# Kernel optimization log

Hardware: AMD Instinct MI355X
Metric: run time of the kernel (lower is better)

Reference implementation:

```python
import jax, jax.numpy as jnp
import numpy as np

N_NODES = 50000
N_EDGES = 1000000
H_DIM = 128
OUT_DIM = 64
N_RELS = 16  # num_bases == num_rels


def setup_inputs() -> dict:
    key = jax.random.key(0)
    ks = jax.random.split(key, 12)
    node_ids = jnp.arange(N_NODES, dtype=jnp.int64) if jax.config.jax_enable_x64 else jnp.arange(N_NODES, dtype=jnp.int32)
    src = jax.random.randint(ks[0], (N_EDGES,), 0, N_NODES)
    dst = jax.random.randint(ks[1], (N_EDGES,), 0, N_NODES)
    etype = jax.random.randint(ks[2], (N_EDGES,), 0, N_RELS)
    norm = jax.random.uniform(ks[3], (N_EDGES, 1), dtype=jnp.float32)
    s1 = 1.0 / np.sqrt(H_DIM)
    s2 = 1.0 / np.sqrt(OUT_DIM)
    emb = jax.random.normal(ks[4], (N_NODES, H_DIM), dtype=jnp.float32)
    V1 = jax.random.normal(ks[5], (N_RELS, H_DIM, H_DIM), dtype=jnp.float32) * s1
    comp1 = jax.random.normal(ks[6], (N_RELS, N_RELS), dtype=jnp.float32) * (1.0 / np.sqrt(N_RELS))
    bias1 = jnp.zeros((H_DIM,), dtype=jnp.float32)
    V2 = jax.random.normal(ks[7], (N_RELS, H_DIM, OUT_DIM), dtype=jnp.float32) * s2
    comp2 = jax.random.normal(ks[8], (N_RELS, N_RELS), dtype=jnp.float32) * (1.0 / np.sqrt(N_RELS))
    bias2 = jnp.zeros((OUT_DIM,), dtype=jnp.float32)
    return {"node_ids": node_ids, "src": src, "dst": dst, "etype": etype, "norm": norm,
            "emb": emb, "V1": V1, "comp1": comp1, "bias1": bias1,
            "V2": V2, "comp2": comp2, "bias2": bias2}


def _rel_graph_conv(x, src, dst, etype, norm, V, comp, bias, num_nodes):
    # Basis decomposition: W_r = sum_b comp[r, b] * V_b  -> [R, in, out]
    W = jnp.einsum('rb,bio->rio', comp, V)
    # Per-relation transform of all nodes: [R, N, out]
    Y = jnp.einsum('ni,rio->rno', x, W)
    # Per-edge message: gather (etype, src) then scale by norm  -> [E, out]
    m = Y[etype, src] * norm
    # Scatter-add to destination nodes
    h = jax.ops.segment_sum(m, dst, num_segments=num_nodes)
    return h + bias


def reference(node_ids, src, dst, etype, norm, emb, V1, comp1, bias1, V2, comp2, bias2):
    x = emb[node_ids]  # [N, H]
    h = jax.nn.relu(_rel_graph_conv(x, src, dst, etype, norm, V1, comp1, bias1, x.shape[0]))
    h = _rel_graph_conv(h, src, dst, etype, norm, V2, comp2, bias2, x.shape[0])
    return h
```

## Files before the change

kernel.cpp:

```cpp
#include <hip/hip_runtime.h>


typedef short bf16x8 __attribute__((ext_vector_type(8)));
typedef float f32x4 __attribute__((ext_vector_type(4)));

#define RELS 16
#define HDIM 128
#define DSTBLK 66
#define MT_P 5
#define CHUNK 32
#define MAXBINS 12288
#define MAXCH 96

__device__ inline unsigned short f2bf(float f) {
  unsigned int u = __float_as_uint(f);
  unsigned int r = u + 0x7FFFu + ((u >> 16) & 1u);
  return (unsigned short)(r >> 16);
}

__device__ inline void barrier_nodrain() {
  __builtin_amdgcn_sched_barrier(0);
  asm volatile("s_waitcnt lgkmcnt(0)" ::: "memory");
  __builtin_amdgcn_s_barrier();
  __builtin_amdgcn_sched_barrier(0);
}

__global__ void cvt_bf16(const float* __restrict__ in, unsigned short* __restrict__ out, int n8) {
  int i = blockIdx.x * blockDim.x + threadIdx.x;
  if (i >= n8) return;
  float4 a = ((const float4*)in)[i * 2];
  float4 b = ((const float4*)in)[i * 2 + 1];
  uint4 o;
  o.x = (unsigned)f2bf(a.x) | ((unsigned)f2bf(a.y) << 16);
  o.y = (unsigned)f2bf(a.z) | ((unsigned)f2bf(a.w) << 16);
  o.z = (unsigned)f2bf(b.x) | ((unsigned)f2bf(b.y) << 16);
  o.w = (unsigned)f2bf(b.z) | ((unsigned)f2bf(b.w) << 16);
  ((uint4*)out)[i] = o;
}

__global__ void compute_w(const float* __restrict__ comp, const float* __restrict__ V,
                          unsigned short* __restrict__ Wt, int IO) {
  int idx = blockIdx.x * blockDim.x + threadIdx.x;
  if (idx >= RELS * IO * HDIM) return;
  int k = idx & (HDIM - 1);
  int o = (idx >> 7) % IO;
  int r = idx / (IO * HDIM);
  float s = 0.f;
#pragma unroll
  for (int b = 0; b < RELS; b++)
    s = fmaf(comp[r * RELS + b], V[(size_t)b * HDIM * IO + (size_t)k * IO + o], s);
  Wt[idx] = f2bf(s);
}

__global__ void hist_bins(const int* __restrict__ dst, const int* __restrict__ etype,
                          int n, int nbins, int* __restrict__ counts) {
  __shared__ int lh[MAXBINS];
  for (int j = threadIdx.x; j < nbins; j += blockDim.x) lh[j] = 0;
  __syncthreads();
  for (int i = blockIdx.x * blockDim.x + threadIdx.x; i < n; i += gridDim.x * blockDim.x)
    atomicAdd(&lh[(dst[i] / DSTBLK) * RELS + etype[i]], 1);
  __syncthreads();
  for (int j = threadIdx.x; j < nbins; j += blockDim.x) {
    int c = lh[j];
    if (c) atomicAdd(&counts[j], c);
  }
}

__global__ void scan_offsets(const int* __restrict__ counts, int* __restrict__ offsets, int nbins) {
  __shared__ int csum[256];
  const int t = threadIdx.x;
  const int CH = (nbins + 255) / 256;
  int lo = t * CH, hi = min(lo + CH, nbins);
  int s = 0;
  for (int i = lo; i < hi; i++) s += (counts[i] + 15) & ~15;
  csum[t] = s;
  __syncthreads();
#pragma unroll
  for (int d = 1; d < 256; d <<= 1) {
    int v = (t >= d) ? csum[t - d] : 0;
    __syncthreads();
    csum[t] += v;
    __syncthreads();
  }
  int run = (t == 0) ? 0 : csum[t - 1];
  for (int i = lo; i < hi; i++) {
    offsets[i] = run;
    run += (counts[i] + 15) & ~15;
  }
  if (lo < nbins && hi == nbins) offsets[nbins] = run;
}

__global__ void scatter_bins(const int* __restrict__ src, const int* __restrict__ dst,
                             const int* __restrict__ etype, const float* __restrict__ norm,
                             int n, const int* __restrict__ offsets, int* __restrict__ cursor,
                             uint2* __restrict__ ebuf) {
  for (int i = blockIdx.x * blockDim.x + threadIdx.x; i < n; i += gridDim.x * blockDim.x) {
    int d = dst[i];
    int blk = d / DSTBLK;
    int b = blk * RELS + etype[i];
    int p = offsets[b] + atomicAdd(&cursor[b], 1);
    ebuf[p] = make_uint2((unsigned)src[i] | ((unsigned)(d - blk * DSTBLK) << 20),
                         __float_as_uint(norm[i]));
  }
}

template <int OUT, bool BF16_RELU_OUT>
__launch_bounds__(256, 3)
__global__ void rgcn_layer(const unsigned short* __restrict__ Xb,
                           const unsigned short* __restrict__ Wt,
                           const uint2* __restrict__ ebuf,
                           const int* __restrict__ offsets, const int* __restrict__ counts,
                           const float* __restrict__ bias, void* __restrict__ Hout,
                           int nNodes) {
  constexpr int NT = OUT / 64;
  __shared__ __align__(16) unsigned short xs[2][CHUNK][136];
  __shared__ __align__(16) unsigned short ys[OUT][40];
  __shared__ __align__(16) unsigned short pmat[2][80][40];
  __shared__ __align__(16) int4 descS[MAXCH];
  __shared__ int sBase[16], sCnt[16], sStart[17];

  const int t = threadIdx.x;
  const int w = t >> 6;
  const int lane = t & 63;
  const int quad = lane >> 4;
  const int l16 = lane & 15;
  const int r0 = t >> 4;
  const int k8 = t & 15;
  const bool isHandler = (t & 7) == 0;
  const int myCol = t >> 3;
  const int nodeBase = blockIdx.x * DSTBLK;
  const int binBase = blockIdx.x * RELS;
  const int colBase = w * (OUT / 4);

  for (int i = t; i < 2 * CHUNK * 136 / 8; i += 256) ((uint4*)xs)[i] = make_uint4(0, 0, 0, 0);
  for (int i = t; i < OUT * 40 / 8; i += 256) ((uint4*)ys)[i] = make_uint4(0, 0, 0, 0);
  for (int i = t; i < 2 * 80 * 40 / 8; i += 256) ((uint4*)pmat)[i] = make_uint4(0, 0, 0, 0);

  if (t < 16) {
    sBase[t] = offsets[binBase + t];
    sCnt[t] = counts[binBase + t];
  }
  __syncthreads();
  if (t == 0) {
    int run = 0;
#pragma unroll
    for (int b = 0; b < 16; b++) {
      sStart[b] = run;
      run += (sCnt[b] + CHUNK - 1) / CHUNK;
    }
    sStart[16] = min(run, MAXCH);
  }
  __syncthreads();
  if (t < 16) {
    int st = sStart[t], ba = sBase[t], c = sCnt[t];
    for (int j = 0; j * CHUNK < c; j++)
      if (st + j < MAXCH)
        descS[st + j] = make_int4(ba + j * CHUNK, min(CHUNK, c - j * CHUNK), t, 0);
  }
  __syncthreads();
  const int nCh = sStart[16];

  f32x4 pacc[MT_P][NT] = {};

  uint2 EnE0, EnE1, EnEm;
  uint2 En2E0, En2E1, En2Em;
  uint4 GnG0, GnG1;
  int n1 = 0, n2 = 0;
  int pdA = -1, pdB = -1;

  if (nCh > 0) {
    int4 d0 = descS[0];
    int4 d1 = (nCh > 1) ? descS[1] : make_int4(0, 0, 0, 0);
    int4 d2 = (nCh > 2) ? descS[2] : make_int4(0, 0, 0, 0);
    n1 = d1.y;
    n2 = d2.y;
    uint2 a0, a1, am;
    if (r0 < d0.y) a0 = ebuf[d0.x + r0];
    if (16 + r0 < d0.y) a1 = ebuf[d0.x + 16 + r0];
    if (isHandler && myCol < d0.y) am = ebuf[d0.x + myCol];
    if (r0 < n1) EnE0 = ebuf[d1.x + r0];
    if (16 + r0 < n1) EnE1 = ebuf[d1.x + 16 + r0];
    if (isHandler && myCol < n1) EnEm = ebuf[d1.x + myCol];
    if (r0 < n2) En2E0 = ebuf[d2.x + r0];
    if (16 + r0 < n2) En2E1 = ebuf[d2.x + 16 + r0];
    if (isHandler && myCol < n2) En2Em = ebuf[d2.x + myCol];
    if (r0 < d0.y)
      *(uint4*)&xs[0][r0][k8 * 8] =
          *(const uint4*)(Xb + (size_t)(a0.x & 0xFFFFFu) * HDIM + k8 * 8);
    if (16 + r0 < d0.y)
      *(uint4*)&xs[0][16 + r0][k8 * 8] =
          *(const uint4*)(Xb + (size_t)(a1.x & 0xFFFFFu) * HDIM + k8 * 8);
    if (isHandler && myCol < d0.y) {
      int dl = (int)(am.x >> 20) & 127;
      pmat[0][dl][myCol] = f2bf(__uint_as_float(am.y));
      pdB = dl;
    }
    if (r0 < n1) GnG0 = *(const uint4*)(Xb + (size_t)(EnE0.x & 0xFFFFFu) * HDIM + k8 * 8);
    if (16 + r0 < n1) GnG1 = *(const uint4*)(Xb + (size_t)(EnE1.x & 0xFFFFFu) * HDIM + k8 * 8);
  }
  barrier_nodrain();

  int cb = 0;
  int curRel = -1;
  bf16x8 wf[4][NT];

  for (int ci = 0; ci < nCh; ci++) {
    int4 dc = descS[ci];
    const int nRows = dc.y;

    if (dc.z != curRel) {
      curRel = dc.z;
      const unsigned short* Wr = Wt + (size_t)curRel * OUT * HDIM;
#pragma unroll
      for (int ks = 0; ks < 4; ks++)
#pragma unroll
        for (int nt = 0; nt < NT; nt++)
          wf[ks][nt] = *(const bf16x8*)(Wr + (size_t)(colBase + nt * 16 + l16) * HDIM + ks * 32 + quad * 8);
    }

    int4 d3 = make_int4(0, 0, 0, 0);
    if (ci + 3 < nCh) d3 = descS[ci + 3];
    uint2 EwE0, EwE1, EwEm;
    if (r0 < d3.y) EwE0 = ebuf[d3.x + r0];
    if (16 + r0 < d3.y) EwE1 = ebuf[d3.x + 16 + r0];
    if (isHandler && myCol < d3.y) EwEm = ebuf[d3.x + myCol];

#pragma unroll
    for (int mt = 0; mt < 2; mt++) {
      if (mt * 16 < nRows) {
        f32x4 dacc[NT] = {};
        __builtin_amdgcn_s_setprio(1);
#pragma unroll
        for (int ks = 0; ks < 4; ks++) {
          bf16x8 a = *(const bf16x8*)&xs[cb][mt * 16 + l16][ks * 32 + quad * 8];
#pragma unroll
          for (int nt = 0; nt < NT; nt++)
            dacc[nt] = __builtin_amdgcn_mfma_f32_16x16x32_bf16(a, wf[ks][nt], dacc[nt], 0, 0, 0);
        }
        __builtin_amdgcn_s_setprio(0);
#pragma unroll
        for (int nt = 0; nt < NT; nt++) {
          uint2 pk;
          pk.x = (unsigned)f2bf(dacc[nt][0]) | ((unsigned)f2bf(dacc[nt][1]) << 16);
          pk.y = (unsigned)f2bf(dacc[nt][2]) | ((unsigned)f2bf(dacc[nt][3]) << 16);
          *(uint2*)&ys[colBase + nt * 16 + l16][mt * 16 + quad * 4] = pk;
        }
      }
    }

    uint4 GwG0, GwG1;
    if (r0 < n2) GwG0 = *(const uint4*)(Xb + (size_t)(En2E0.x & 0xFFFFFu) * HDIM + k8 * 8);
    if (16 + r0 < n2) GwG1 = *(const uint4*)(Xb + (size_t)(En2E1.x & 0xFFFFFu) * HDIM + k8 * 8);

    {
      bf16x8 bfv[NT];
#pragma unroll
      for (int nt = 0; nt < NT; nt++)
        bfv[nt] = *(const bf16x8*)&ys[colBase + nt * 16 + l16][quad * 8];
      __builtin_amdgcn_s_setprio(1);
#pragma unroll
      for (int mt = 0; mt < MT_P; mt++) {
        bf16x8 a = *(const bf16x8*)&pmat[cb][mt * 16 + l16][quad * 8];
#pragma unroll
        for (int nt = 0; nt < NT; nt++)
          pacc[mt][nt] = __builtin_amdgcn_mfma_f32_16x16x32_bf16(a, bfv[nt], pacc[mt][nt], 0, 0, 0);
      }
      __builtin_amdgcn_s_setprio(0);
    }

    if (r0 < n1) *(uint4*)&xs[cb ^ 1][r0][k8 * 8] = GnG0;
    if (16 + r0 < n1) *(uint4*)&xs[cb ^ 1][16 + r0][k8 * 8] = GnG1;
    if (isHandler) {
      if (pdA >= 0) pmat[cb ^ 1][pdA][myCol] = 0;
      if (myCol < n1) {
        int dl = (int)(EnEm.x >> 20) & 127;
        pmat[cb ^ 1][dl][myCol] = f2bf(__uint_as_float(EnEm.y));
        pdA = dl;
      } else {
        pdA = -1;
      }
    }
    { int tmp = pdA; pdA = pdB; pdB = tmp; }

    EnE0 = En2E0; EnE1 = En2E1; EnEm = En2Em;
    En2E0 = EwE0; En2E1 = EwE1; En2Em = EwEm;
    GnG0 = GwG0; GnG1 = GwG1;
    n1 = n2; n2 = d3.y;

    if (ci + 1 < nCh) barrier_nodrain();
    cb ^= 1;
  }

#pragma unroll
  for (int mt = 0; mt < MT_P; mt++) {
#pragma unroll
    for (int reg = 0; reg < 4; reg++) {
      int ld = mt * 16 + quad * 4 + reg;
      int node = nodeBase + ld;
      if (ld < DSTBLK && node < nNodes) {
#pragma unroll
        for (int nt = 0; nt < NT; nt++) {
          int col = colBase + nt * 16 + l16;
          float v = pacc[mt][nt][reg] + bias[col];
          if constexpr (BF16_RELU_OUT)
            ((unsigned short*)Hout)[(size_t)node * OUT + col] = f2bf(fmaxf(v, 0.f));
          else
            ((float*)Hout)[(size_t)node * OUT + col] = v;
        }
      }
    }
  }
}

extern "C" void kernel_launch(void* const* d_in, const int* in_sizes, int n_in,
                              void* d_out, int out_size, void* d_ws, size_t ws_size,
                              hipStream_t stream) {
  const int*   src   = (const int*)d_in[1];
  const int*   dst   = (const int*)d_in[2];
  const int*   etype = (const int*)d_in[3];
  const float* norm  = (const float*)d_in[4];
  const float* emb   = (const float*)d_in[5];
  const float* V1    = (const float*)d_in[6];
  const float* comp1 = (const float*)d_in[7];
  const float* bias1 = (const float*)d_in[8];
  const float* V2    = (const float*)d_in[9];
  const float* comp2 = (const float*)d_in[10];
  const float* bias2 = (const float*)d_in[11];
  float* out = (float*)d_out;

  const int N = in_sizes[0];
  const int E = in_sizes[1];
  const int H = 128, O = 64;
  const int NB = (N + DSTBLK - 1) / DSTBLK;
  const int NBINS = NB * RELS;
  const int EPAD_MAX = E + NBINS * 16;

  char* ws = (char*)d_ws;
  size_t off = 0;
  auto alloc = [&](size_t bytes) -> void* {
    void* p = ws + off;
    off += (bytes + 255) & ~(size_t)255;
    return p;
  };
  unsigned short* W1t  = (unsigned short*)alloc(sizeof(short) * RELS * H * H);
  unsigned short* W2t  = (unsigned short*)alloc(sizeof(short) * RELS * O * H);
  unsigned short* embh = (unsigned short*)alloc(sizeof(short) * (size_t)N * H);
  unsigned short* h1b  = (unsigned short*)alloc(sizeof(short) * (size_t)N * H);
  uint2* ebuf = (uint2*)alloc(sizeof(uint2) * EPAD_MAX);
  int* counts  = (int*)alloc(sizeof(int) * NBINS);
  int* cursor  = (int*)alloc(sizeof(int) * NBINS);
  int* offsets = (int*)alloc(sizeof(int) * (NBINS + 1));

  hipMemsetAsync(counts, 0, sizeof(int) * NBINS, stream);
  hipMemsetAsync(cursor, 0, sizeof(int) * NBINS, stream);

  cvt_bf16<<<((size_t)N * H / 8 + 255) / 256, 256, 0, stream>>>(emb, embh, N * H / 8);
  compute_w<<<(RELS * H * H + 255) / 256, 256, 0, stream>>>(comp1, V1, W1t, H);
  compute_w<<<(RELS * O * H + 255) / 256, 256, 0, stream>>>(comp2, V2, W2t, O);
  hist_bins<<<256, 256, 0, stream>>>(dst, etype, E, NBINS, counts);
  scan_offsets<<<1, 256, 0, stream>>>(counts, offsets, NBINS);
  scatter_bins<<<1024, 256, 0, stream>>>(src, dst, etype, norm, E, offsets, cursor, ebuf);

  rgcn_layer<128, true><<<NB, 256, 0, stream>>>(embh, W1t, ebuf, offsets, counts, bias1, (void*)h1b, N);
  rgcn_layer<64, false><<<NB, 256, 0, stream>>>(h1b, W2t, ebuf, offsets, counts, bias2, (void*)out, N);
}
```

Measured before the change: 420.4 us.

## Replace scatter-matrix MFMA with LDS float atomics for per-edge accumulation

The kernel no longer builds a bf16 one-hot norm matrix and runs a second MFMA to scatter per-edge messages onto destination nodes. It keeps the per-edge transform results in registers and adds them, scaled by norm, into an fp32 LDS output tile with shared-memory atomics. The output tile is then written out with vectorized stores that fold in bias and ReLU. Together with the launch-bounds change this drops the zero-initialisation and bf16 round trip of the intermediate and keeps fp32 accumulation, at the cost of many LDS atomics and possible contention on popular destinations.

Measured after the change: 1.334 ms. 217% more time.

```diff
diff --git a/kernel.cpp b/kernel.cpp
--- a/kernel.cpp
+++ b/kernel.cpp
@@ -7,7 +7,6 @@
 #define RELS 16
 #define HDIM 128
 #define DSTBLK 66
-#define MT_P 5
 #define CHUNK 32
 #define MAXBINS 12288
 #define MAXCH 96
@@ -105,7 +104,7 @@
 }
 
 template <int OUT, bool BF16_RELU_OUT>
-__launch_bounds__(256, 3)
+__launch_bounds__(256, (OUT == 64) ? 4 : 3)
 __global__ void rgcn_layer(const unsigned short* __restrict__ Xb,
                            const unsigned short* __restrict__ Wt,
                            const uint2* __restrict__ ebuf,
@@ -113,10 +112,12 @@
                            const float* __restrict__ bias, void* __restrict__ Hout,
                            int nNodes) {
   constexpr int NT = OUT / 64;
+  constexpr int OSTR = OUT + 4;
   __shared__ __align__(16) unsigned short xs[2][CHUNK][136];
-  __shared__ __align__(16) unsigned short ys[OUT][40];
-  __shared__ __align__(16) unsigned short pmat[2][80][40];
-  __shared__ __align__(16) int4 descS[MAXCH];
+  __shared__ __align__(16) float lds_out[DSTBLK * OSTR];
+  __shared__ __align__(16) float normS[2][CHUNK];
+  __shared__ __align__(4) unsigned char dlocS[2][CHUNK];
+  __shared__ __align__(8) int2 descS[MAXCH];
   __shared__ int sBase[16], sCnt[16], sStart[17];
 
   const int t = threadIdx.x;
@@ -126,15 +127,11 @@
   const int l16 = lane & 15;
   const int r0 = t >> 4;
   const int k8 = t & 15;
-  const bool isHandler = (t & 7) == 0;
-  const int myCol = t >> 3;
   const int nodeBase = blockIdx.x * DSTBLK;
   const int binBase = blockIdx.x * RELS;
   const int colBase = w * (OUT / 4);
 
-  for (int i = t; i < 2 * CHUNK * 136 / 8; i += 256) ((uint4*)xs)[i] = make_uint4(0, 0, 0, 0);
-  for (int i = t; i < OUT * 40 / 8; i += 256) ((uint4*)ys)[i] = make_uint4(0, 0, 0, 0);
-  for (int i = t; i < 2 * 80 * 40 / 8; i += 256) ((uint4*)pmat)[i] = make_uint4(0, 0, 0, 0);
+  for (int i = t; i < DSTBLK * OSTR / 4; i += 256) ((uint4*)lds_out)[i] = make_uint4(0, 0, 0, 0);
 
   if (t < 16) {
     sBase[t] = offsets[binBase + t];
@@ -155,45 +152,45 @@
     int st = sStart[t], ba = sBase[t], c = sCnt[t];
     for (int j = 0; j * CHUNK < c; j++)
       if (st + j < MAXCH)
-        descS[st + j] = make_int4(ba + j * CHUNK, min(CHUNK, c - j * CHUNK), t, 0);
+        descS[st + j] = make_int2(ba + j * CHUNK, min(CHUNK, c - j * CHUNK) | (t << 8));
   }
   __syncthreads();
   const int nCh = sStart[16];
 
-  f32x4 pacc[MT_P][NT] = {};
-
-  uint2 EnE0, EnE1, EnEm;
-  uint2 En2E0, En2E1, En2Em;
+  uint2 EnE0, EnE1;
+  uint2 En2E0, En2E1;
   uint4 GnG0, GnG1;
   int n1 = 0, n2 = 0;
-  int pdA = -1, pdB = -1;
 
   if (nCh > 0) {
-    int4 d0 = descS[0];
-    int4 d1 = (nCh > 1) ? descS[1] : make_int4(0, 0, 0, 0);
-    int4 d2 = (nCh > 2) ? descS[2] : make_int4(0, 0, 0, 0);
-    n1 = d1.y;
-    n2 = d2.y;
-    uint2 a0, a1, am;
-    if (r0 < d0.y) a0 = ebuf[d0.x + r0];
-    if (16 + r0 < d0.y) a1 = ebuf[d0.x + 16 + r0];
-    if (isHandler && myCol < d0.y) am = ebuf[d0.x + myCol];
+    int2 d0 = descS[0];
+    int2 d1 = (nCh > 1) ? descS[1] : make_int2(0, 0);
+    int2 d2 = (nCh > 2) ? descS[2] : make_int2(0, 0);
+    const int rows0 = d0.y & 0xFF;
+    n1 = d1.y & 0xFF;
+    n2 = d2.y & 0xFF;
+    uint2 a0, a1;
+    if (r0 < rows0) a0 = ebuf[d0.x + r0];
+    if (16 + r0 < rows0) a1 = ebuf[d0.x + 16 + r0];
     if (r0 < n1) EnE0 = ebuf[d1.x + r0];
     if (16 + r0 < n1) EnE1 = ebuf[d1.x + 16 + r0];
-    if (isHandler && myCol < n1) EnEm = ebuf[d1.x + myCol];
     if (r0 < n2) En2E0 = ebuf[d2.x + r0];
     if (16 + r0 < n2) En2E1 = ebuf[d2.x + 16 + r0];
-    if (isHandler && myCol < n2) En2Em = ebuf[d2.x + myCol];
-    if (r0 < d0.y)
+    if (r0 < rows0) {
       *(uint4*)&xs[0][r0][k8 * 8] =
           *(const uint4*)(Xb + (size_t)(a0.x & 0xFFFFFu) * HDIM + k8 * 8);
-    if (16 + r0 < d0.y)
+      if (k8 == 0) {
+        dlocS[0][r0] = (unsigned char)((a0.x >> 20) & 127u);
+        normS[0][r0] = __uint_as_float(a0.y);
+      }
+    }
+    if (16 + r0 < rows0) {
       *(uint4*)&xs[0][16 + r0][k8 * 8] =
           *(const uint4*)(Xb + (size_t)(a1.x & 0xFFFFFu) * HDIM + k8 * 8);
-    if (isHandler && myCol < d0.y) {
-      int dl = (int)(am.x >> 20) & 127;
-      pmat[0][dl][myCol] = f2bf(__uint_as_float(am.y));
-      pdB = dl;
+      if (k8 == 0) {
+        dlocS[0][16 + r0] = (unsigned char)((a1.x >> 20) & 127u);
+        normS[0][16 + r0] = __uint_as_float(a1.y);
+      }
     }
     if (r0 < n1) GnG0 = *(const uint4*)(Xb + (size_t)(EnE0.x & 0xFFFFFu) * HDIM + k8 * 8);
     if (16 + r0 < n1) GnG1 = *(const uint4*)(Xb + (size_t)(EnE1.x & 0xFFFFFu) * HDIM + k8 * 8);
@@ -205,12 +202,13 @@
   bf16x8 wf[4][NT];
 
   for (int ci = 0; ci < nCh; ci++) {
-    int4 dc = descS[ci];
-    const int nRows = dc.y;
-
-    if (dc.z != curRel) {
-      curRel = dc.z;
-      const unsigned short* Wr = Wt + (size_t)curRel * OUT * HDIM;
+    int2 dc = descS[ci];
+    const int nRows = dc.y & 0xFF;
+    const int rel = dc.y >> 8;
+
+    if (rel != curRel) {
+      curRel = rel;
+      const unsigned short* Wr = Wt + (size_t)rel * OUT * HDIM;
 #pragma unroll
       for (int ks = 0; ks < 4; ks++)
 #pragma unroll
@@ -218,33 +216,28 @@
           wf[ks][nt] = *(const bf16x8*)(Wr + (size_t)(colBase + nt * 16 + l16) * HDIM + ks * 32 + quad * 8);
     }
 
-    int4 d3 = make_int4(0, 0, 0, 0);
+    int2 d3 = make_int2(0, 0);
     if (ci + 3 < nCh) d3 = descS[ci + 3];
-    uint2 EwE0, EwE1, EwEm;
-    if (r0 < d3.y) EwE0 = ebuf[d3.x + r0];
-    if (16 + r0 < d3.y) EwE1 = ebuf[d3.x + 16 + r0];
-    if (isHandler && myCol < d3.y) EwEm = ebuf[d3.x + myCol];
-
+    const int rows3 = d3.y & 0xFF;
+    uint2 EwE0, EwE1;
+    if (r0 < rows3) EwE0 = ebuf[d3.x + r0];
+    if (16 + r0 < rows3) EwE1 = ebuf[d3.x + 16 + r0];
+
+    f32x4 dacc[2][NT];
 #pragma unroll
     for (int mt = 0; mt < 2; mt++) {
+#pragma unroll
+      for (int nt = 0; nt < NT; nt++) dacc[mt][nt] = (f32x4){0.f, 0.f, 0.f, 0.f};
       if (mt * 16 < nRows) {
-        f32x4 dacc[NT] = {};
         __builtin_amdgcn_s_setprio(1);
 #pragma unroll
         for (int ks = 0; ks < 4; ks++) {
           bf16x8 a = *(const bf16x8*)&xs[cb][mt * 16 + l16][ks * 32 + quad * 8];
 #pragma unroll
           for (int nt = 0; nt < NT; nt++)
-            dacc[nt] = __builtin_amdgcn_mfma_f32_16x16x32_bf16(a, wf[ks][nt], dacc[nt], 0, 0, 0);
+            dacc[mt][nt] = __builtin_amdgcn_mfma_f32_16x16x32_bf16(a, wf[ks][nt], dacc[mt][nt], 0, 0, 0);
         }
         __builtin_amdgcn_s_setprio(0);
-#pragma unroll
-        for (int nt = 0; nt < NT; nt++) {
-          uint2 pk;
-          pk.x = (unsigned)f2bf(dacc[nt][0]) | ((unsigned)f2bf(dacc[nt][1]) << 16);
-          pk.y = (unsigned)f2bf(dacc[nt][2]) | ((unsigned)f2bf(dacc[nt][3]) << 16);
-          *(uint2*)&ys[colBase + nt * 16 + l16][mt * 16 + quad * 4] = pk;
-        }
       }
     }
 
@@ -252,61 +245,76 @@
     if (r0 < n2) GwG0 = *(const uint4*)(Xb + (size_t)(En2E0.x & 0xFFFFFu) * HDIM + k8 * 8);
     if (16 + r0 < n2) GwG1 = *(const uint4*)(Xb + (size_t)(En2E1.x & 0xFFFFFu) * HDIM + k8 * 8);
 
-    {
-      bf16x8 bfv[NT];
-#pragma unroll
-      for (int nt = 0; nt < NT; nt++)
-        bfv[nt] = *(const bf16x8*)&ys[colBase + nt * 16 + l16][quad * 8];
-      __builtin_amdgcn_s_setprio(1);
-#pragma unroll
-      for (int mt = 0; mt < MT_P; mt++) {
-        bf16x8 a = *(const bf16x8*)&pmat[cb][mt * 16 + l16][quad * 8];
-#pragma unroll
-        for (int nt = 0; nt < NT; nt++)
-          pacc[mt][nt] = __builtin_amdgcn_mfma_f32_16x16x32_bf16(a, bfv[nt], pacc[mt][nt], 0, 0, 0);
-      }
-      __builtin_amdgcn_s_setprio(0);
-    }
-
-    if (r0 < n1) *(uint4*)&xs[cb ^ 1][r0][k8 * 8] = GnG0;
-    if (16 + r0 < n1) *(uint4*)&xs[cb ^ 1][16 + r0][k8 * 8] = GnG1;
-    if (isHandler) {
-      if (pdA >= 0) pmat[cb ^ 1][pdA][myCol] = 0;
-      if (myCol < n1) {
-        int dl = (int)(EnEm.x >> 20) & 127;
-        pmat[cb ^ 1][dl][myCol] = f2bf(__uint_as_float(EnEm.y));
-        pdA = dl;
-      } else {
-        pdA = -1;
-      }
-    }
-    { int tmp = pdA; pdA = pdB; pdB = tmp; }
-
-    EnE0 = En2E0; EnE1 = En2E1; EnEm = En2Em;
-    En2E0 = EwE0; En2E1 = EwE1; En2Em = EwEm;
+#pragma unroll
+    for (int mt = 0; mt < 2; mt++) {
+      if (mt * 16 < nRows) {
+        unsigned dl4 = *(const unsigned*)&dlocS[cb][mt * 16 + quad * 4];
+        f32x4 nv = *(const f32x4*)&normS[cb][mt * 16 + quad * 4];
+#pragma unroll
+        for (int reg = 0; reg < 4; reg++) {
+          int row = mt * 16 + quad * 4 + reg;
+          if (row < nRows) {
+            int dloc = (int)((dl4 >> (8 * reg)) & 127u);
+            float nm = nv[reg];
+#pragma unroll
+            for (int nt = 0; nt < NT; nt++)
+              atomicAdd(&lds_out[dloc * OSTR + colBase + nt * 16 + l16],
+                        dacc[mt][nt][reg] * nm);
+          }
+        }
+      }
+    }
+
+    if (r0 < n1) {
+      *(uint4*)&xs[cb ^ 1][r0][k8 * 8] = GnG0;
+      if (k8 == 0) {
+        dlocS[cb ^ 1][r0] = (unsigned char)((EnE0.x >> 20) & 127u);
+        normS[cb ^ 1][r0] = __uint_as_float(EnE0.y);
+      }
+    }
+    if (16 + r0 < n1) {
+      *(uint4*)&xs[cb ^ 1][16 + r0][k8 * 8] = GnG1;
+      if (k8 == 0) {
+        dlocS[cb ^ 1][16 + r0] = (unsigned char)((EnE1.x >> 20) & 127u);
+        normS[cb ^ 1][16 + r0] = __uint_as_float(EnE1.y);
+      }
+    }
+
+    EnE0 = En2E0; EnE1 = En2E1;
+    En2E0 = EwE0; En2E1 = EwE1;
     GnG0 = GwG0; GnG1 = GwG1;
-    n1 = n2; n2 = d3.y;
+    n1 = n2; n2 = rows3;
 
     if (ci + 1 < nCh) barrier_nodrain();
     cb ^= 1;
   }
 
-#pragma unroll
-  for (int mt = 0; mt < MT_P; mt++) {
-#pragma unroll
-    for (int reg = 0; reg < 4; reg++) {
-      int ld = mt * 16 + quad * 4 + reg;
-      int node = nodeBase + ld;
-      if (ld < DSTBLK && node < nNodes) {
-#pragma unroll
-        for (int nt = 0; nt < NT; nt++) {
-          int col = colBase + nt * 16 + l16;
-          float v = pacc[mt][nt][reg] + bias[col];
-          if constexpr (BF16_RELU_OUT)
-            ((unsigned short*)Hout)[(size_t)node * OUT + col] = f2bf(fmaxf(v, 0.f));
-          else
-            ((float*)Hout)[(size_t)node * OUT + col] = v;
-        }
+  __syncthreads();
+
+  if (BF16_RELU_OUT) {
+#pragma unroll 2
+    for (int i = t; i < DSTBLK * (OUT / 4); i += 256) {
+      int node = i / (OUT / 4);
+      int col4 = (i % (OUT / 4)) * 4;
+      if (nodeBase + node < nNodes) {
+        f32x4 v = *(const f32x4*)&lds_out[node * OSTR + col4];
+        float4 b = *(const float4*)&bias[col4];
+        uint2 pk;
+        pk.x = (unsigned)f2bf(fmaxf(v[0] + b.x, 0.f)) | ((unsigned)f2bf(fmaxf(v[1] + b.y, 0.f)) << 16);
+        pk.y = (unsigned)f2bf(fmaxf(v[2] + b.z, 0.f)) | ((unsigned)f2bf(fmaxf(v[3] + b.w, 0.f)) << 16);
+        *(uint2*)&((unsigned short*)Hout)[(size_t)(nodeBase + node) * OUT + col4] = pk;
+      }
+    }
+  } else {
+#pragma unroll 2
+    for (int i = t; i < DSTBLK * (OUT / 4); i += 256) {
+      int node = i / (OUT / 4);
+      int col4 = (i % (OUT / 4)) * 4;
+      if (nodeBase + node < nNodes) {
+        f32x4 v = *(const f32x4*)&lds_out[node * OSTR + col4];
+        float4 b = *(const float4*)&bias[col4];
+        float4 o = make_float4(v[0] + b.x, v[1] + b.y, v[2] + b.z, v[3] + b.w);
+        *(float4*)&((float*)Hout)[(size_t)(nodeBase + node) * OUT + col4] = o;
       }
     }
   }
```

## Load gathered source rows directly into MFMA A-fragments, drop LDS staging buffer

Applied to the files above, without the earlier changes.

Gathered source-node feature rows are now loaded straight from global memory into per-lane MFMA A-operand registers, replacing the double-buffered xs shared-memory staging and its writes and reads. The chunk descriptor is packed from int4 into int2, and the OUT=64 variant gets a higher minimum-occupancy launch bound. This cuts LDS traffic and footprint to allow more resident blocks, at the cost of more registers per thread and a shorter prefetch depth for gathers (one chunk ahead instead of two), which may expose gather latency or cause spills.

Result: slower. 573.4 us (+36.4%).

```diff
diff --git a/kernel.cpp b/kernel.cpp
--- a/kernel.cpp
+++ b/kernel.cpp
@@ -105,7 +105,7 @@
 }
 
 template <int OUT, bool BF16_RELU_OUT>
-__launch_bounds__(256, 3)
+__launch_bounds__(256, (OUT == 64) ? 4 : 3)
 __global__ void rgcn_layer(const unsigned short* __restrict__ Xb,
                            const unsigned short* __restrict__ Wt,
                            const uint2* __restrict__ ebuf,
@@ -113,10 +113,9 @@
                            const float* __restrict__ bias, void* __restrict__ Hout,
                            int nNodes) {
   constexpr int NT = OUT / 64;
-  __shared__ __align__(16) unsigned short xs[2][CHUNK][136];
   __shared__ __align__(16) unsigned short ys[OUT][40];
   __shared__ __align__(16) unsigned short pmat[2][80][40];
-  __shared__ __align__(16) int4 descS[MAXCH];
+  __shared__ __align__(8) int2 descS[MAXCH];
   __shared__ int sBase[16], sCnt[16], sStart[17];
 
   const int t = threadIdx.x;
@@ -124,15 +123,12 @@
   const int lane = t & 63;
   const int quad = lane >> 4;
   const int l16 = lane & 15;
-  const int r0 = t >> 4;
-  const int k8 = t & 15;
   const bool isHandler = (t & 7) == 0;
   const int myCol = t >> 3;
   const int nodeBase = blockIdx.x * DSTBLK;
   const int binBase = blockIdx.x * RELS;
   const int colBase = w * (OUT / 4);
 
-  for (int i = t; i < 2 * CHUNK * 136 / 8; i += 256) ((uint4*)xs)[i] = make_uint4(0, 0, 0, 0);
   for (int i = t; i < OUT * 40 / 8; i += 256) ((uint4*)ys)[i] = make_uint4(0, 0, 0, 0);
   for (int i = t; i < 2 * 80 * 40 / 8; i += 256) ((uint4*)pmat)[i] = make_uint4(0, 0, 0, 0);
 
@@ -155,48 +151,50 @@
     int st = sStart[t], ba = sBase[t], c = sCnt[t];
     for (int j = 0; j * CHUNK < c; j++)
       if (st + j < MAXCH)
-        descS[st + j] = make_int4(ba + j * CHUNK, min(CHUNK, c - j * CHUNK), t, 0);
+        descS[st + j] = make_int2(ba + j * CHUNK, min(CHUNK, c - j * CHUNK) | (t << 8));
   }
   __syncthreads();
   const int nCh = sStart[16];
 
   f32x4 pacc[MT_P][NT] = {};
 
-  uint2 EnE0, EnE1, EnEm;
-  uint2 En2E0, En2E1, En2Em;
-  uint4 GnG0, GnG1;
-  int n1 = 0, n2 = 0;
+  bf16x8 Af[2][4];
+  uint2 Erow[2];
+  uint2 EnEm, En2Em;
+  int n1 = 0;
   int pdA = -1, pdB = -1;
 
   if (nCh > 0) {
-    int4 d0 = descS[0];
-    int4 d1 = (nCh > 1) ? descS[1] : make_int4(0, 0, 0, 0);
-    int4 d2 = (nCh > 2) ? descS[2] : make_int4(0, 0, 0, 0);
-    n1 = d1.y;
-    n2 = d2.y;
-    uint2 a0, a1, am;
-    if (r0 < d0.y) a0 = ebuf[d0.x + r0];
-    if (16 + r0 < d0.y) a1 = ebuf[d0.x + 16 + r0];
-    if (isHandler && myCol < d0.y) am = ebuf[d0.x + myCol];
-    if (r0 < n1) EnE0 = ebuf[d1.x + r0];
-    if (16 + r0 < n1) EnE1 = ebuf[d1.x + 16 + r0];
-    if (isHandler && myCol < n1) EnEm = ebuf[d1.x + myCol];
-    if (r0 < n2) En2E0 = ebuf[d2.x + r0];
-    if (16 + r0 < n2) En2E1 = ebuf[d2.x + 16 + r0];
-    if (isHandler && myCol < n2) En2Em = ebuf[d2.x + myCol];
-    if (r0 < d0.y)
-      *(uint4*)&xs[0][r0][k8 * 8] =
-          *(const uint4*)(Xb + (size_t)(a0.x & 0xFFFFFu) * HDIM + k8 * 8);
-    if (16 + r0 < d0.y)
-      *(uint4*)&xs[0][16 + r0][k8 * 8] =
-          *(const uint4*)(Xb + (size_t)(a1.x & 0xFFFFFu) * HDIM + k8 * 8);
-    if (isHandler && myCol < d0.y) {
+    int2 d0 = descS[0];
+    int2 d1 = (nCh > 1) ? descS[1] : make_int2(0, 0);
+    int2 d2 = (nCh > 2) ? descS[2] : make_int2(0, 0);
+    const int rows0 = d0.y & 0xFF;
+    n1 = d1.y & 0xFF;
+    const int rows2 = d2.y & 0xFF;
+    uint2 E0[2];
+#pragma unroll
+    for (int mt = 0; mt < 2; mt++) {
+      int row = mt * 16 + l16;
+      E0[mt] = ebuf[d0.x + min(row, rows0 - 1)];
+      if (n1 > 0) Erow[mt] = ebuf[d1.x + min(row, n1 - 1)];
+    }
+    uint2 am;
+    if (isHandler) {
+      if (myCol < rows0) am = ebuf[d0.x + myCol];
+      if (myCol < n1) EnEm = ebuf[d1.x + myCol];
+      if (myCol < rows2) En2Em = ebuf[d2.x + myCol];
+    }
+#pragma unroll
+    for (int mt = 0; mt < 2; mt++) {
+      const unsigned short* p = Xb + (size_t)(E0[mt].x & 0xFFFFFu) * HDIM + quad * 8;
+#pragma unroll
+      for (int ks = 0; ks < 4; ks++) Af[mt][ks] = *(const bf16x8*)(p + ks * 32);
+    }
+    if (isHandler && myCol < rows0) {
       int dl = (int)(am.x >> 20) & 127;
       pmat[0][dl][myCol] = f2bf(__uint_as_float(am.y));
       pdB = dl;
     }
-    if (r0 < n1) GnG0 = *(const uint4*)(Xb + (size_t)(EnE0.x & 0xFFFFFu) * HDIM + k8 * 8);
-    if (16 + r0 < n1) GnG1 = *(const uint4*)(Xb + (size_t)(EnE1.x & 0xFFFFFu) * HDIM + k8 * 8);
   }
   barrier_nodrain();
 
@@ -205,12 +203,13 @@
   bf16x8 wf[4][NT];
 
   for (int ci = 0; ci < nCh; ci++) {
-    int4 dc = descS[ci];
-    const int nRows = dc.y;
-
-    if (dc.z != curRel) {
-      curRel = dc.z;
-      const unsigned short* Wr = Wt + (size_t)curRel * OUT * HDIM;
+    int2 dc = descS[ci];
+    const int nRows = dc.y & 0xFF;
+    const int rel = dc.y >> 8;
+
+    if (rel != curRel) {
+      curRel = rel;
+      const unsigned short* Wr = Wt + (size_t)rel * OUT * HDIM;
 #pragma unroll
       for (int ks = 0; ks < 4; ks++)
 #pragma unroll
@@ -218,12 +217,18 @@
           wf[ks][nt] = *(const bf16x8*)(Wr + (size_t)(colBase + nt * 16 + l16) * HDIM + ks * 32 + quad * 8);
     }
 
-    int4 d3 = make_int4(0, 0, 0, 0);
-    if (ci + 3 < nCh) d3 = descS[ci + 3];
-    uint2 EwE0, EwE1, EwEm;
-    if (r0 < d3.y) EwE0 = ebuf[d3.x + r0];
-    if (16 + r0 < d3.y) EwE1 = ebuf[d3.x + 16 + r0];
-    if (isHandler && myCol < d3.y) EwEm = ebuf[d3.x + myCol];
+    int2 d2 = (ci + 2 < nCh) ? descS[ci + 2] : make_int2(0, 0);
+    int2 d3 = (ci + 3 < nCh) ? descS[ci + 3] : make_int2(0, 0);
+    const int n2 = d2.y & 0xFF;
+    const int n3 = d3.y & 0xFF;
+    uint2 ErowN[2];
+    if (n2 > 0) {
+#pragma unroll
+      for (int mt = 0; mt < 2; mt++)
+        ErowN[mt] = ebuf[d2.x + min(mt * 16 + l16, n2 - 1)];
+    }
+    uint2 EwEm;
+    if (isHandler && myCol < n3) EwEm = ebuf[d3.x + myCol];
 
 #pragma unroll
     for (int mt = 0; mt < 2; mt++) {
@@ -232,10 +237,9 @@
         __builtin_amdgcn_s_setprio(1);
 #pragma unroll
         for (int ks = 0; ks < 4; ks++) {
-          bf16x8 a = *(const bf16x8*)&xs[cb][mt * 16 + l16][ks * 32 + quad * 8];
 #pragma unroll
           for (int nt = 0; nt < NT; nt++)
-            dacc[nt] = __builtin_amdgcn_mfma_f32_16x16x32_bf16(a, wf[ks][nt], dacc[nt], 0, 0, 0);
+            dacc[nt] = __builtin_amdgcn_mfma_f32_16x16x32_bf16(Af[mt][ks], wf[ks][nt], dacc[nt], 0, 0, 0);
         }
         __builtin_amdgcn_s_setprio(0);
 #pragma unroll
@@ -248,9 +252,14 @@
       }
     }
 
-    uint4 GwG0, GwG1;
-    if (r0 < n2) GwG0 = *(const uint4*)(Xb + (size_t)(En2E0.x & 0xFFFFFu) * HDIM + k8 * 8);
-    if (16 + r0 < n2) GwG1 = *(const uint4*)(Xb + (size_t)(En2E1.x & 0xFFFFFu) * HDIM + k8 * 8);
+    if (n1 > 0) {
+#pragma unroll
+      for (int mt = 0; mt < 2; mt++) {
+        const unsigned short* p = Xb + (size_t)(Erow[mt].x & 0xFFFFFu) * HDIM + quad * 8;
+#pragma unroll
+        for (int ks = 0; ks < 4; ks++) Af[mt][ks] = *(const bf16x8*)(p + ks * 32);
+      }
+    }
 
     {
       bf16x8 bfv[NT];
@@ -268,8 +277,6 @@
       __builtin_amdgcn_s_setprio(0);
     }
 
-    if (r0 < n1) *(uint4*)&xs[cb ^ 1][r0][k8 * 8] = GnG0;
-    if (16 + r0 < n1) *(uint4*)&xs[cb ^ 1][16 + r0][k8 * 8] = GnG1;
     if (isHandler) {
       if (pdA >= 0) pmat[cb ^ 1][pdA][myCol] = 0;
       if (myCol < n1) {
@@ -282,10 +289,9 @@
     }
     { int tmp = pdA; pdA = pdB; pdB = tmp; }
 
-    EnE0 = En2E0; EnE1 = En2E1; EnEm = En2Em;
-    En2E0 = EwE0; En2E1 = EwE1; En2Em = EwEm;
-    GnG0 = GwG0; GnG1 = GwG1;
-    n1 = n2; n2 = d3.y;
+    Erow[0] = ErowN[0]; Erow[1] = ErowN[1];
+    EnEm = En2Em; En2Em = EwEm;
+    n1 = n2;
 
     if (ci + 1 < nCh) barrier_nodrain();
     cb ^= 1;
```
